# Optimization experiments

Measured on AMD Instinct MI355X. Metric: run time of the kernel, lower is better.

The kernel has to match this reference:

```python
import jax, jax.numpy as jnp
import numpy as np

DMODEL, Q_HEADS, KV_HEADS, SEQ_LEN = 4096, 32, 8, 2048
HEAD_DIM = DMODEL // Q_HEADS  # 128
ROPE_BASE = 500000.0


def _rope_sin_cos(head_dim, length, base):
    # Faithful numpy port of LlamaRoPE.__init__ (llama3 frequency scaling).
    freqs = 1.0 / np.power(base, np.arange(0, head_dim, 2, dtype=np.float64) / head_dim)
    factor, low_ff, high_ff, old_ctx = 32.0, 1.0, 4.0, 8192.0
    low_wl, high_wl = old_ctx / low_ff, old_ctx / high_ff
    wavelen = 2.0 * np.pi / freqs
    inv = np.where(wavelen > low_wl, freqs / factor, freqs)
    smooth = (old_ctx / wavelen - low_ff) / (high_ff - low_ff)
    smoothed = (1.0 - smooth) * inv / factor + smooth * inv
    is_medium = (~(wavelen < high_wl)) & (~(wavelen > low_wl))
    inv = np.where(is_medium, smoothed, inv)
    angles = np.arange(length, dtype=np.float64)[:, None] * inv[None, :]  # [S, D/2]
    angles = np.concatenate([angles, angles], axis=-1)  # repeat(1,2) -> [S, D]
    return (jnp.asarray(np.sin(angles), jnp.float32),
            jnp.asarray(np.cos(angles), jnp.float32))


def _apply_rope(x, sin, cos):
    # x: [B, H, S, D]; sin/cos: [S, D]
    half = x.shape[-1] // 2
    rot = jnp.concatenate([-x[..., half:], x[..., :half]], axis=-1)
    return x * cos[None, None] + rot * sin[None, None]


def setup_inputs() -> dict:
    key = jax.random.key(0)
    kx, kq, kk, kv, ko = jax.random.split(key, 5)
    s = 0.02
    return {
        "x": jax.random.normal(kx, (2, SEQ_LEN, DMODEL), jnp.float32),
        "wq": jax.random.normal(kq, (DMODEL, DMODEL), jnp.float32) * s,
        "wk": jax.random.normal(kk, (KV_HEADS * HEAD_DIM, DMODEL), jnp.float32) * s,
        "wv": jax.random.normal(kv, (KV_HEADS * HEAD_DIM, DMODEL), jnp.float32) * s,
        "wo": jax.random.normal(ko, (DMODEL, DMODEL), jnp.float32) * s,
    }


def reference(x, wq, wk, wv, wo):
    B, S, _ = x.shape
    sin, cos = _rope_sin_cos(HEAD_DIM, SEQ_LEN, ROPE_BASE)
    # projections (nn.Linear: y = x @ W.T)
    q = (x @ wq.T).reshape(B, S, Q_HEADS, HEAD_DIM).transpose(0, 2, 1, 3)
    k = (x @ wk.T).reshape(B, S, KV_HEADS, HEAD_DIM).transpose(0, 2, 1, 3)
    v = (x @ wv.T).reshape(B, S, KV_HEADS, HEAD_DIM).transpose(0, 2, 1, 3)
    q = _apply_rope(q, sin, cos)
    k = _apply_rope(k, sin, cos)
    # GQA repeat_kv: [B, KV, S, D] -> [B, Q, S, D]
    rep = Q_HEADS // KV_HEADS
    k = jnp.repeat(k, rep, axis=1)
    v = jnp.repeat(v, rep, axis=1)
    # causal SDPA
    scale = 1.0 / jnp.sqrt(jnp.asarray(HEAD_DIM, jnp.float32))
    scores = jnp.einsum("bhqd,bhkd->bhqk", q, k) * scale
    mask = jnp.tril(jnp.ones((S, S), dtype=bool))
    scores = jnp.where(mask[None, None], scores, jnp.asarray(-jnp.inf, scores.dtype))
    attn = jax.nn.softmax(scores, axis=-1)
    out = jnp.einsum("bhqk,bhkd->bhqd", attn, v)
    out = out.transpose(0, 2, 1, 3).reshape(B, S, DMODEL)
    return out @ wo.T
```

## Files before the change

kernel.cpp:

```cpp
#include <hip/hip_runtime.h>
#include <cstdint>

#define S_LEN 2048
#define DM 4096
#define NQH 32
#define NKVH 8
#define HD 128

typedef __bf16 bf16x8 __attribute__((ext_vector_type(8)));
typedef float f32x4 __attribute__((ext_vector_type(4)));
typedef unsigned short u16;
typedef unsigned short u16x8 __attribute__((ext_vector_type(8)));
typedef unsigned int u32;

__device__ __forceinline__ float bf2f(u16 h) {
  union { u32 u; float f; } v; v.u = ((u32)h) << 16; return v.f;
}
__device__ __forceinline__ u16 f2bf(float f) {
  union { float f; u32 u; } v; v.f = f;
  u32 u = v.u;
  return (u16)((u + 0x7FFFu + ((u >> 16) & 1u)) >> 16);
}

__device__ __forceinline__ void gload16(const void* g, const void* l) {
  __builtin_amdgcn_global_load_lds(
      (const __attribute__((address_space(1))) u32*)(uintptr_t)g,
      (__attribute__((address_space(3))) u32*)(u32)(uintptr_t)l,
      16, 0, 0);
}

__device__ __forceinline__ void stage16(const float* __restrict__ g, u16* l) {
  const float4* gp = reinterpret_cast<const float4*>(g);
  float4 v0 = gp[0], v1 = gp[1], v2 = gp[2], v3 = gp[3];
  u16x8 a, b;
  a[0] = f2bf(v0.x); a[1] = f2bf(v0.y); a[2] = f2bf(v0.z); a[3] = f2bf(v0.w);
  a[4] = f2bf(v1.x); a[5] = f2bf(v1.y); a[6] = f2bf(v1.z); a[7] = f2bf(v1.w);
  b[0] = f2bf(v2.x); b[1] = f2bf(v2.y); b[2] = f2bf(v2.z); b[3] = f2bf(v2.w);
  b[4] = f2bf(v3.x); b[5] = f2bf(v3.y); b[6] = f2bf(v3.z); b[7] = f2bf(v3.w);
  *reinterpret_cast<u16x8*>(l) = a;
  *reinterpret_cast<u16x8*>(l + 8) = b;
}
__device__ __forceinline__ void stage16(const u16* __restrict__ g, u16* l) {
  *reinterpret_cast<u16x8*>(l) = *reinterpret_cast<const u16x8*>(g);
  *reinterpret_cast<u16x8*>(l + 8) = *reinterpret_cast<const u16x8*>(g + 8);
}

__device__ __forceinline__ void stc(u16* p, float v) { *p = f2bf(v); }
__device__ __forceinline__ void stc(float* p, float v) { *p = v; }

__device__ __forceinline__ void cvt8(const float* in, u16* out, size_t i8) {
  const float4* gp = reinterpret_cast<const float4*>(in) + i8 * 2;
  float4 a = gp[0], b = gp[1];
  u16x8 o;
  o[0] = f2bf(a.x); o[1] = f2bf(a.y); o[2] = f2bf(a.z); o[3] = f2bf(a.w);
  o[4] = f2bf(b.x); o[5] = f2bf(b.y); o[6] = f2bf(b.z); o[7] = f2bf(b.w);
  reinterpret_cast<u16x8*>(out)[i8] = o;
}
__global__ void cvt_all(const float* x, const float* wq, const float* wk,
                        const float* wv, const float* wo,
                        u16* xb, u16* wqkvb, u16* wob) {
  const size_t NX8 = (size_t)2 * S_LEN * DM / 8;
  const size_t NW8 = (size_t)DM * DM / 8;
  const size_t NK8 = (size_t)NKVH * HD * DM / 8;
  const size_t total = NX8 + NW8 + 2 * NK8 + NW8;
  size_t stride = (size_t)gridDim.x * blockDim.x;
  for (size_t i = (size_t)blockIdx.x * blockDim.x + threadIdx.x; i < total; i += stride) {
    if (i < NX8)                       cvt8(x,  xb,                    i);
    else if (i < NX8 + NW8)            cvt8(wq, wqkvb,                 i - NX8);
    else if (i < NX8 + NW8 + NK8)      cvt8(wk, wqkvb + NW8 * 8,       i - NX8 - NW8);
    else if (i < NX8 + NW8 + 2 * NK8)  cvt8(wv, wqkvb + (NW8 + NK8) * 8, i - NX8 - NW8 - NK8);
    else                               cvt8(wo, wob,                   i - NX8 - NW8 - 2 * NK8);
  }
}

__global__ void rope_table_kernel(float* __restrict__ sin_t, float* __restrict__ cos_t) {
  int idx = blockIdx.x * blockDim.x + threadIdx.x;
  if (idx >= S_LEN * 64) return;
  int s = idx >> 6, i = idx & 63;
  const double PI = 3.14159265358979323846;
  double freq = pow(500000.0, -((double)i) / 64.0);
  double wavelen = 2.0 * PI / freq;
  double inv = (wavelen > 8192.0) ? freq / 32.0 : freq;
  if (!(wavelen < 2048.0) && !(wavelen > 8192.0)) {
    double smooth = (8192.0 / wavelen - 1.0) / 3.0;
    inv = (1.0 - smooth) * (freq / 32.0) + smooth * freq;
  }
  double ang = (double)s * inv;
  sin_t[idx] = (float)sin(ang);
  cos_t[idx] = (float)cos(ang);
}

__global__ void rope_apply(u16* __restrict__ X, const float* __restrict__ sin_t,
                           const float* __restrict__ cos_t, float scale, int nrows) {
  int idx = blockIdx.x * blockDim.x + threadIdx.x;
  if (idx >= nrows * 64) return;
  int row = idx >> 6, i = idx & 63;
  int s = row & (S_LEN - 1);
  size_t base = (size_t)row * HD;
  float lo = bf2f(X[base + i]);
  float hi = bf2f(X[base + i + 64]);
  float sn = sin_t[s * 64 + i];
  float cs = cos_t[s * 64 + i];
  X[base + i] = f2bf((lo * cs - hi * sn) * scale);
  X[base + i + 64] = f2bf((hi * cs + lo * sn) * scale);
}

template <int MODE, typename TC>
__global__ __launch_bounds__(256, 4)
void gemm16(const u16* __restrict__ A, const u16* __restrict__ B,
            TC* __restrict__ C, int M, int N, int K, int H) {
  __shared__ u16 sA[128 * 64];
  __shared__ u16 sB[128 * 64];
  const int tid = threadIdx.x;
  const int lane = tid & 63;
  const int wv = tid >> 6;
  const int wr = wv >> 1, wc = wv & 1;
  const int bm = blockIdx.y * 128;
  const int bn = blockIdx.x * 128;
  const int fr = lane & 15, fq = lane >> 4;
  const int srow_base = wv * 8 + (lane >> 3);
  const int sgran = (((lane & 7) ^ ((lane >> 3) & 7))) * 8;
  const int rxor = fr & 7;

  f32x4 zero4 = {0.f, 0.f, 0.f, 0.f};
  f32x4 acc[4][4];
#pragma unroll
  for (int i = 0; i < 4; ++i)
#pragma unroll
    for (int j = 0; j < 4; ++j) acc[i][j] = zero4;

  for (int k0 = 0; k0 < K; k0 += 64) {
    __syncthreads();
#pragma unroll
    for (int g = 0; g < 4; ++g) {
      int row = g * 32 + srow_base;
      gload16(A + (size_t)(bm + row) * K + k0 + sgran, sA + g * 2048 + wv * 512);
      gload16(B + (size_t)(bn + row) * K + k0 + sgran, sB + g * 2048 + wv * 512);
    }
    __syncthreads();
#pragma unroll
    for (int kk = 0; kk < 2; ++kk) {
      bf16x8 af[4], bg[4];
      const int gofs = ((kk * 4 + fq) ^ rxor) * 8;
#pragma unroll
      for (int i = 0; i < 4; ++i) {
        af[i] = *(const bf16x8*)(sA + (wr * 64 + i * 16 + fr) * 64 + gofs);
        bg[i] = *(const bf16x8*)(sB + (wc * 64 + i * 16 + fr) * 64 + gofs);
      }
#pragma unroll
      for (int i = 0; i < 4; ++i)
#pragma unroll
        for (int j = 0; j < 4; ++j)
          acc[i][j] = __builtin_amdgcn_mfma_f32_16x16x32_bf16(af[i], bg[j], acc[i][j], 0, 0, 0);
    }
  }

#pragma unroll
  for (int i = 0; i < 4; ++i)
#pragma unroll
    for (int j = 0; j < 4; ++j)
#pragma unroll
      for (int r = 0; r < 4; ++r) {
        int m = bm + wr * 64 + i * 16 + fq * 4 + r;
        int n = bn + wc * 64 + j * 16 + fr;
        stc(C + (size_t)m * N + n, acc[i][j][r]);
      }
}

__global__ __launch_bounds__(256, 4)
void gemm_qkv(const u16* __restrict__ A, const u16* __restrict__ B,
              u16* __restrict__ Cq, u16* __restrict__ Ck, u16* __restrict__ Cv,
              int K) {
  __shared__ u16 sA[128 * 64];
  __shared__ u16 sB[128 * 64];
  const int tid = threadIdx.x;
  const int lane = tid & 63;
  const int wv = tid >> 6;
  const int wr = wv >> 1, wc = wv & 1;
  const int bm = blockIdx.y * 128;
  const int bn = blockIdx.x * 128;
  const int fr = lane & 15, fq = lane >> 4;
  const int srow_base = wv * 8 + (lane >> 3);
  const int sgran = (((lane & 7) ^ ((lane >> 3) & 7))) * 8;
  const int rxor = fr & 7;

  f32x4 zero4 = {0.f, 0.f, 0.f, 0.f};
  f32x4 acc[4][4];
#pragma unroll
  for (int i = 0; i < 4; ++i)
#pragma unroll
    for (int j = 0; j < 4; ++j) acc[i][j] = zero4;

  for (int k0 = 0; k0 < K; k0 += 64) {
    __syncthreads();
#pragma unroll
    for (int g = 0; g < 4; ++g) {
      int row = g * 32 + srow_base;
      gload16(A + (size_t)(bm + row) * K + k0 + sgran, sA + g * 2048 + wv * 512);
      gload16(B + (size_t)(bn + row) * K + k0 + sgran, sB + g * 2048 + wv * 512);
    }
    __syncthreads();
#pragma unroll
    for (int kk = 0; kk < 2; ++kk) {
      bf16x8 af[4], bg[4];
      const int gofs = ((kk * 4 + fq) ^ rxor) * 8;
#pragma unroll
      for (int i = 0; i < 4; ++i) {
        af[i] = *(const bf16x8*)(sA + (wr * 64 + i * 16 + fr) * 64 + gofs);
        bg[i] = *(const bf16x8*)(sB + (wc * 64 + i * 16 + fr) * 64 + gofs);
      }
#pragma unroll
      for (int i = 0; i < 4; ++i)
#pragma unroll
        for (int j = 0; j < 4; ++j)
          acc[i][j] = __builtin_amdgcn_mfma_f32_16x16x32_bf16(af[i], bg[j], acc[i][j], 0, 0, 0);
    }
  }

#pragma unroll
  for (int i = 0; i < 4; ++i)
#pragma unroll
    for (int j = 0; j < 4; ++j)
#pragma unroll
      for (int r = 0; r < 4; ++r) {
        int m = bm + wr * 64 + i * 16 + fq * 4 + r;
        int n = bn + wc * 64 + j * 16 + fr;
        int b = m >> 11, s = m & 2047;
        u16 hval = f2bf(acc[i][j][r]);
        if (n < 4096) {
          int hh = n >> 7, d = n & 127;
          Cq[(((size_t)(b * NQH + hh)) * S_LEN + s) * HD + d] = hval;
        } else if (n < 5120) {
          int nn = n - 4096;
          int hh = nn >> 7, d = nn & 127;
          Ck[(((size_t)(b * NKVH + hh)) * S_LEN + s) * HD + d] = hval;
        } else {
          int nn = n - 5120;
          int hh = nn >> 7, d = nn & 127;
          Cv[(((size_t)(b * NKVH + hh)) * HD + d) * S_LEN + s] = hval;
        }
      }
}

template <int MODE, typename TA, typename TB, typename TC>
__global__ __launch_bounds__(256, 2)
void gemm_bt(const TA* __restrict__ A, const TB* __restrict__ B,
             TC* __restrict__ C, int M, int N, int K, int H) {
  __shared__ u16 sA[128 * 32];
  __shared__ u16 sB[128 * 32];
  const int tid = threadIdx.x;
  const int lane = tid & 63;
  const int wv = tid >> 6;
  const int wr = wv >> 1, wc = wv & 1;
  const int bm = blockIdx.y * 128;
  const int bn = blockIdx.x * 128;
  const int fr = lane & 15, fq = lane >> 4;
  const int srow = tid >> 1;
  const int shalf = (tid & 1) * 16;

  f32x4 zero4 = {0.f, 0.f, 0.f, 0.f};
  f32x4 acc[4][4];
#pragma unroll
  for (int i = 0; i < 4; ++i)
#pragma unroll
    for (int j = 0; j < 4; ++j) acc[i][j] = zero4;

  for (int k0 = 0; k0 < K; k0 += 32) {
    __syncthreads();
    stage16(A + (size_t)(bm + srow) * K + k0 + shalf, sA + srow * 32 + shalf);
    stage16(B + (size_t)(bn + srow) * K + k0 + shalf, sB + srow * 32 + shalf);
    __syncthreads();
    bf16x8 af[4], bg[4];
#pragma unroll
    for (int i = 0; i < 4; ++i) {
      af[i] = *(const bf16x8*)(sA + (wr * 64 + i * 16 + fr) * 32 + fq * 8);
      bg[i] = *(const bf16x8*)(sB + (wc * 64 + i * 16 + fr) * 32 + fq * 8);
    }
#pragma unroll
    for (int i = 0; i < 4; ++i)
#pragma unroll
      for (int j = 0; j < 4; ++j)
        acc[i][j] = __builtin_amdgcn_mfma_f32_16x16x32_bf16(af[i], bg[j], acc[i][j], 0, 0, 0);
  }

#pragma unroll
  for (int i = 0; i < 4; ++i)
#pragma unroll
    for (int j = 0; j < 4; ++j)
#pragma unroll
      for (int r = 0; r < 4; ++r) {
        int m = bm + wr * 64 + i * 16 + fq * 4 + r;
        int n = bn + wc * 64 + j * 16 + fr;
        float v = acc[i][j][r];
        if (MODE == 0) {
          stc(C + (size_t)m * N + n, v);
        } else if (MODE == 1) {
          int b = m >> 11, s = m & 2047, hh = n >> 7, d = n & 127;
          stc(C + (((size_t)(b * H + hh)) * S_LEN + s) * HD + d, v);
        } else {
          int b = m >> 11, s = m & 2047, hh = n >> 7, d = n & 127;
          stc(C + (((size_t)(b * H + hh)) * HD + d) * S_LEN + s, v);
        }
      }
}

__global__ __launch_bounds__(256, 2)
void attn_kernel(const u16* __restrict__ Q, const u16* __restrict__ K,
                 const u16* __restrict__ V, u16* __restrict__ O,
                 const float* __restrict__ sin_t, const float* __restrict__ cos_t,
                 float scale) {
  __shared__ u16 sK[64 * 128];
  __shared__ u16 sV[128 * 64];
  __shared__ u16 sP[4][16 * 64];

  const int tid = threadIdx.x, lane = tid & 63, wv = tid >> 6;
  const int fr = lane & 15, fq = lane >> 4;
  const int bx = blockIdx.x;
  const int bh = blockIdx.y;
  const int b = bh >> 5, h = bh & 31;
  const int hkv = h >> 2;
  const u16* Qb = Q + (size_t)bh * S_LEN * HD;
  const u16* Kb = K + (size_t)(b * NKVH + hkv) * S_LEN * HD;
  const u16* Vb = V + (size_t)(b * NKVH + hkv) * HD * S_LEN;

  for (int half = 0; half < 2; ++half) {
    const int q0 = (half == 0 ? (15 - bx) : bx) * 128;

    u16x8 qfu[2][4];
#pragma unroll
    for (int u = 0; u < 2; ++u) {
      int qrow = q0 + wv * 32 + u * 16 + fr;
      const u16* qp = Qb + (size_t)qrow * HD;
      u16x8 raw[4];
#pragma unroll
      for (int ks = 0; ks < 4; ++ks)
        raw[ks] = *(const u16x8*)(qp + ks * 32 + fq * 8);
#pragma unroll
      for (int p = 0; p < 2; ++p) {
        const float* cb = cos_t + (size_t)qrow * 64 + p * 32 + fq * 8;
        const float* sb = sin_t + (size_t)qrow * 64 + p * 32 + fq * 8;
        float4 c0 = ((const float4*)cb)[0], c1 = ((const float4*)cb)[1];
        float4 s0 = ((const float4*)sb)[0], s1 = ((const float4*)sb)[1];
        float cs[8] = {c0.x, c0.y, c0.z, c0.w, c1.x, c1.y, c1.z, c1.w};
        float sn[8] = {s0.x, s0.y, s0.z, s0.w, s1.x, s1.y, s1.z, s1.w};
#pragma unroll
        for (int j = 0; j < 8; ++j) {
          float lo = bf2f(raw[p][j]);
          float hi = bf2f(raw[p + 2][j]);
          qfu[u][p][j]     = f2bf((lo * cs[j] - hi * sn[j]) * scale);
          qfu[u][p + 2][j] = f2bf((hi * cs[j] + lo * sn[j]) * scale);
        }
      }
    }
    const bf16x8* qf0 = (const bf16x8*)&qfu[0][0];
    const bf16x8* qf1 = (const bf16x8*)&qfu[1][0];

    f32x4 zero4 = {0.f, 0.f, 0.f, 0.f};
    f32x4 o[2][8];
    float m[2][4], l[2][4];
#pragma unroll
    for (int u = 0; u < 2; ++u) {
#pragma unroll
      for (int dt = 0; dt < 8; ++dt) o[u][dt] = zero4;
#pragma unroll
      for (int r = 0; r < 4; ++r) { m[u][r] = -3.0e38f; l[u][r] = 0.f; }
    }

    const int ntiles = (q0 >> 6) + 2;
    for (int t = 0; t < ntiles; ++t) {
      const int s0 = t * 64;
      __syncthreads();
#pragma unroll
      for (int j = 0; j < 4; ++j) {
        int c = j * 4 + wv;
        {
          int row = c * 4 + (lane >> 4);
          int e = ((lane & 15) ^ (row & 7)) * 8;
          gload16(Kb + (size_t)(s0 + row) * HD + e, sK + c * 512);
        }
        {
          int row = c * 8 + (lane >> 3);
          int e = ((lane & 7) ^ (row & 7)) * 8;
          gload16(Vb + (size_t)row * S_LEN + s0 + e, sV + c * 512);
        }
      }
      __syncthreads();

      f32x4 sc[2][4];
#pragma unroll
      for (int u = 0; u < 2; ++u)
#pragma unroll
        for (int j = 0; j < 4; ++j) sc[u][j] = zero4;
      __builtin_amdgcn_s_setprio(1);
#pragma unroll
      for (int j = 0; j < 4; ++j) {
#pragma unroll
        for (int ks = 0; ks < 4; ++ks) {
          int row = j * 16 + fr;
          int e = (ks * 32 + fq * 8) ^ ((row & 7) << 3);
          bf16x8 kf = *(const bf16x8*)(sK + row * 128 + e);
          sc[0][j] = __builtin_amdgcn_mfma_f32_16x16x32_bf16(qf0[ks], kf, sc[0][j], 0, 0, 0);
          sc[1][j] = __builtin_amdgcn_mfma_f32_16x16x32_bf16(qf1[ks], kf, sc[1][j], 0, 0, 0);
        }
      }
      __builtin_amdgcn_s_setprio(0);

      if (t >= ntiles - 2) {
#pragma unroll
        for (int u = 0; u < 2; ++u)
#pragma unroll
          for (int j = 0; j < 4; ++j)
#pragma unroll
            for (int r = 0; r < 4; ++r) {
              int kvp = s0 + j * 16 + fr;
              int qp = q0 + wv * 32 + u * 16 + fq * 4 + r;
              if (kvp > qp) sc[u][j][r] = -3.0e38f;
            }
      }

      bf16x8 pa[2][2];
#pragma unroll
      for (int u = 0; u < 2; ++u) {
        float al[4];
        bool resc = false;
#pragma unroll
        for (int r = 0; r < 4; ++r) {
          float v = fmaxf(fmaxf(sc[u][0][r], sc[u][1][r]), fmaxf(sc[u][2][r], sc[u][3][r]));
          v = fmaxf(v, __shfl_xor(v, 1, 64));
          v = fmaxf(v, __shfl_xor(v, 2, 64));
          v = fmaxf(v, __shfl_xor(v, 4, 64));
          v = fmaxf(v, __shfl_xor(v, 8, 64));
          if (v > m[u][r] + 8.f) {
            al[r] = __expf(m[u][r] - v);
            m[u][r] = v;
            resc = true;
          } else {
            al[r] = 1.f;
          }
        }
#pragma unroll
        for (int r = 0; r < 4; ++r) {
          float rs = 0.f;
          int prow = fq * 4 + r;
#pragma unroll
          for (int j = 0; j < 4; ++j) {
            float pv = __expf(sc[u][j][r] - m[u][r]);
            rs += pv;
            int e = (j * 16 + fr) ^ ((prow & 7) << 3);
            sP[wv][prow * 64 + e] = f2bf(pv);
          }
          l[u][r] = l[u][r] * al[r] + rs;
        }
        if (resc) {
#pragma unroll
          for (int r = 0; r < 4; ++r)
#pragma unroll
            for (int dt = 0; dt < 8; ++dt) o[u][dt][r] *= al[r];
        }
#pragma unroll
        for (int ks = 0; ks < 2; ++ks) {
          int e = (ks * 32 + fq * 8) ^ ((fr & 7) << 3);
          pa[u][ks] = *(const bf16x8*)(&sP[wv][fr * 64 + e]);
        }
      }

      __builtin_amdgcn_s_setprio(1);
#pragma unroll
      for (int dt = 0; dt < 8; ++dt) {
#pragma unroll
        for (int ks = 0; ks < 2; ++ks) {
          int row = dt * 16 + fr;
          int e = (ks * 32 + fq * 8) ^ ((row & 7) << 3);
          bf16x8 vf = *(const bf16x8*)(sV + row * 64 + e);
#pragma unroll
          for (int u = 0; u < 2; ++u)
            o[u][dt] = __builtin_amdgcn_mfma_f32_16x16x32_bf16(pa[u][ks], vf, o[u][dt], 0, 0, 0);
        }
      }
      __builtin_amdgcn_s_setprio(0);
    }

#pragma unroll
    for (int u = 0; u < 2; ++u)
#pragma unroll
      for (int r = 0; r < 4; ++r) {
        float lt = l[u][r];
        lt += __shfl_xor(lt, 1, 64);
        lt += __shfl_xor(lt, 2, 64);
        lt += __shfl_xor(lt, 4, 64);
        lt += __shfl_xor(lt, 8, 64);
        int qp = q0 + wv * 32 + u * 16 + fq * 4 + r;
        float inv_l = 1.0f / lt;
        size_t base = ((size_t)b * S_LEN + qp) * DM + h * HD;
#pragma unroll
        for (int dt = 0; dt < 8; ++dt)
          O[base + dt * 16 + fr] = f2bf(o[u][dt][r] * inv_l);
      }
  }
}

extern "C" void kernel_launch(void* const* d_in, const int* in_sizes, int n_in,
                              void* d_out, int out_size, void* d_ws, size_t ws_size,
                              hipStream_t stream) {
  const float* x  = (const float*)d_in[0];
  const float* wq = (const float*)d_in[1];
  const float* wk = (const float*)d_in[2];
  const float* wv = (const float*)d_in[3];
  const float* wo = (const float*)d_in[4];

  char* ws = (char*)d_ws;
  size_t off = 0;
  auto alloc = [&](size_t bytes) {
    void* p = ws + off;
    off += (bytes + 255) & ~(size_t)255;
    return p;
  };

  const size_t nx  = (size_t)2 * S_LEN * DM;
  const size_t nwq = (size_t)DM * DM;
  const size_t nwk = (size_t)(NKVH * HD) * DM;

  const float scale = 0.08838834764831845f;
  const int nrk = 2 * NKVH * S_LEN;
  dim3 blk(256);

  if (ws_size >= ((size_t)180 << 20)) {
    u16* xb    = (u16*)alloc(nx * 2);
    u16* wqkvb = (u16*)alloc((nwq + 2 * nwk) * 2);
    u16* wob   = (u16*)alloc(nwq * 2);
    u16* qb    = (u16*)alloc(nx * 2);
    u16* kb    = (u16*)alloc(nwk * 2);
    u16* vtb   = (u16*)alloc(nwk * 2);
    float* sin_t = (float*)alloc((size_t)S_LEN * 64 * 4);
    float* cos_t = (float*)alloc((size_t)S_LEN * 64 * 4);
    u16* aob = xb;

    cvt_all<<<2048, 256, 0, stream>>>(x, wq, wk, wv, wo, xb, wqkvb, wob);
    rope_table_kernel<<<(S_LEN * 64 + 255) / 256, 256, 0, stream>>>(sin_t, cos_t);

    gemm_qkv<<<dim3(48, 32), blk, 0, stream>>>(xb, wqkvb, qb, kb, vtb, DM);

    rope_apply<<<((size_t)nrk * 64 + 255) / 256, 256, 0, stream>>>(kb, sin_t, cos_t, 1.0f, nrk);

    attn_kernel<<<dim3(8, 64), blk, 0, stream>>>(qb, kb, vtb, aob, sin_t, cos_t, scale);

    gemm16<0, float><<<dim3(32, 32), blk, 0, stream>>>(aob, wob, (float*)d_out, 4096, DM, DM, 0);
  } else {
    u16* qb  = (u16*)alloc(nx * 2);
    u16* kb  = (u16*)alloc(nwk * 2);
    u16* vtb = (u16*)alloc(nwk * 2);
    u16* aob = (u16*)alloc(nx * 2);
    float* sin_t = (float*)alloc((size_t)S_LEN * 64 * 4);
    float* cos_t = (float*)alloc((size_t)S_LEN * 64 * 4);

    rope_table_kernel<<<(S_LEN * 64 + 255) / 256, 256, 0, stream>>>(sin_t, cos_t);

    gemm_bt<1, float, float, u16><<<dim3(32, 32), blk, 0, stream>>>(x, wq, qb, 4096, DM, DM, NQH);
    gemm_bt<1, float, float, u16><<<dim3(8, 32), blk, 0, stream>>>(x, wk, kb, 4096, 1024, DM, NKVH);
    gemm_bt<2, float, float, u16><<<dim3(8, 32), blk, 0, stream>>>(x, wv, vtb, 4096, 1024, DM, NKVH);

    rope_apply<<<((size_t)nrk * 64 + 255) / 256, 256, 0, stream>>>(kb, sin_t, cos_t, 1.0f, nrk);

    attn_kernel<<<dim3(8, 64), blk, 0, stream>>>(qb, kb, vtb, aob, sin_t, cos_t, scale);

    gemm_bt<0, u16, float, float><<<dim3(32, 32), blk, 0, stream>>>(aob, wo, (float*)d_out, 4096, DM, DM, 0);
  }
}
```

Baseline: 571.5 us.

## Double-buffer K/V tiles in LDS to prefetch the next tile during compute

The attention kernel now allocates two LDS buffers each for K and V. It issues the global-to-LDS load for tile t+1 before computing on tile t, and replaces the two barriers per tile with one barrier at the end of each iteration. The aim is to hide global memory latency behind the QK and PV MFMA work. In exchange, LDS use per block rises from about 40KB to about 72KB, which could reduce occupancy if two blocks per CU no longer fit.

```diff
diff --git a/kernel.cpp b/kernel.cpp
--- a/kernel.cpp
+++ b/kernel.cpp
@@ -309,8 +309,8 @@
                  const u16* __restrict__ V, u16* __restrict__ O,
                  const float* __restrict__ sin_t, const float* __restrict__ cos_t,
                  float scale) {
-  __shared__ u16 sK[64 * 128];
-  __shared__ u16 sV[128 * 64];
+  __shared__ u16 sK[2][64 * 128];
+  __shared__ u16 sV[2][128 * 64];
   __shared__ u16 sP[4][16 * 64];
 
   const int tid = threadIdx.x, lane = tid & 63, wv = tid >> 6;
@@ -323,6 +323,9 @@
   const u16* Kb = K + (size_t)(b * NKVH + hkv) * S_LEN * HD;
   const u16* Vb = V + (size_t)(b * NKVH + hkv) * HD * S_LEN;
 
+  const int krow_l = lane >> 4, ke_l = lane & 15;
+  const int vrow_l = lane >> 3, ve_l = lane & 7;
+
   for (int half = 0; half < 2; ++half) {
     const int q0 = (half == 0 ? (15 - bx) : bx) * 128;
 
@@ -367,24 +370,35 @@
     }
 
     const int ntiles = (q0 >> 6) + 2;
-    for (int t = 0; t < ntiles; ++t) {
-      const int s0 = t * 64;
-      __syncthreads();
+
+    auto STAGE = [&](int buf, int t) {
+      const int s0k = t * 64;
 #pragma unroll
       for (int j = 0; j < 4; ++j) {
         int c = j * 4 + wv;
         {
-          int row = c * 4 + (lane >> 4);
-          int e = ((lane & 15) ^ (row & 7)) * 8;
-          gload16(Kb + (size_t)(s0 + row) * HD + e, sK + c * 512);
+          int row = c * 4 + krow_l;
+          int e = (ke_l ^ (row & 7)) * 8;
+          gload16(Kb + (size_t)(s0k + row) * HD + e, sK[buf] + c * 512);
         }
         {
-          int row = c * 8 + (lane >> 3);
-          int e = ((lane & 7) ^ (row & 7)) * 8;
-          gload16(Vb + (size_t)row * S_LEN + s0 + e, sV + c * 512);
-        }
-      }
-      __syncthreads();
+          int row = c * 8 + vrow_l;
+          int e = (ve_l ^ (row & 7)) * 8;
+          gload16(Vb + (size_t)row * S_LEN + s0k + e, sV[buf] + c * 512);
+        }
+      }
+    };
+
+    STAGE(0, 0);
+    __syncthreads();
+    int cur = 0;
+
+    for (int t = 0; t < ntiles; ++t) {
+      const int s0 = t * 64;
+      if (t + 1 < ntiles) STAGE(cur ^ 1, t + 1);
+
+      const u16* sKc = sK[cur];
+      const u16* sVc = sV[cur];
 
       f32x4 sc[2][4];
 #pragma unroll
@@ -398,7 +412,7 @@
         for (int ks = 0; ks < 4; ++ks) {
           int row = j * 16 + fr;
           int e = (ks * 32 + fq * 8) ^ ((row & 7) << 3);
-          bf16x8 kf = *(const bf16x8*)(sK + row * 128 + e);
+          bf16x8 kf = *(const bf16x8*)(sKc + row * 128 + e);
           sc[0][j] = __builtin_amdgcn_mfma_f32_16x16x32_bf16(qf0[ks], kf, sc[0][j], 0, 0, 0);
           sc[1][j] = __builtin_amdgcn_mfma_f32_16x16x32_bf16(qf1[ks], kf, sc[1][j], 0, 0, 0);
         }
@@ -471,13 +485,16 @@
         for (int ks = 0; ks < 2; ++ks) {
           int row = dt * 16 + fr;
           int e = (ks * 32 + fq * 8) ^ ((row & 7) << 3);
-          bf16x8 vf = *(const bf16x8*)(sV + row * 64 + e);
+          bf16x8 vf = *(const bf16x8*)(sVc + row * 64 + e);
 #pragma unroll
           for (int u = 0; u < 2; ++u)
             o[u][dt] = __builtin_amdgcn_mfma_f32_16x16x32_bf16(pa[u][ks], vf, o[u][dt], 0, 0, 0);
         }
       }
       __builtin_amdgcn_s_setprio(0);
+
+      __syncthreads();
+      cur ^= 1;
     }
 
 #pragma unroll
```

Measured after the change: 573.0 us (median of 2 runs). No clear change (+0.3%).
